# Kernel tuning notes

Measured on AMD Instinct MI355X. Metric: run time of the kernel, lower is better.

## Reference

```python
import jax, jax.numpy as jnp
import numpy as np

HIDDEN = 1024
N_HEAD = 16
LN_EPS = 1e-5


def _layernorm(x, g, b):
    m = jnp.mean(x, axis=-1, keepdims=True)
    v = jnp.var(x, axis=-1, keepdims=True)
    return (x - m) * jax.lax.rsqrt(v + LN_EPS) * g + b


def setup_inputs() -> dict:
    key = jax.random.key(0)
    ks = jax.random.split(key, 16)
    H = HIDDEN
    s = 0.02
    d = dict(
        x=jax.random.normal(ks[0], (4, 1024, H), jnp.float32),
        Wq=jax.random.normal(ks[1], (H, H), jnp.float32) * s,
        bq=jnp.zeros((H,), jnp.float32),
        Wk=jax.random.normal(ks[2], (H, H), jnp.float32) * s,
        bk=jnp.zeros((H,), jnp.float32),
        Wv=jax.random.normal(ks[3], (H, H), jnp.float32) * s,
        bv=jnp.zeros((H,), jnp.float32),
        Wo=jax.random.normal(ks[4], (H, H), jnp.float32) * s,
        bo=jnp.zeros((H,), jnp.float32),
        g1=jax.random.normal(ks[5], (H,), jnp.float32) * s,
        b1=jnp.zeros((H,), jnp.float32),
        W1=jax.random.normal(ks[6], (H, 4 * H), jnp.float32) * s,
        c1=jnp.zeros((4 * H,), jnp.float32),
        W2=jax.random.normal(ks[7], (4 * H, H), jnp.float32) * s,
        c2=jnp.zeros((H,), jnp.float32),
        g2=jax.random.normal(ks[8], (H,), jnp.float32) * s,
        b2=jnp.zeros((H,), jnp.float32),
    )
    return d


def reference(x, Wq, bq, Wk, bk, Wv, bv, Wo, bo, g1, b1, W1, c1, W2, c2, g2, b2):
    N, T, Hd = x.shape
    Hh = N_HEAD
    D = Hd // Hh
    # faithful to torch code: .view(N, H, T, D) is a raw reshape, no transpose
    q = (x @ Wq + bq).reshape(N, Hh, T, D)
    k = (x @ Wk + bk).reshape(N, Hh, T, D)
    v = (x @ Wv + bv).reshape(N, Hh, T, D)
    scores = jnp.einsum('nhtd,nhsd->nhts', q, k) / jnp.sqrt(jnp.float32(Hd))
    # faithful: softmax over dim=1 (the head axis)
    attn = jax.nn.softmax(scores, axis=1)
    o = jnp.einsum('nhts,nhsd->nhtd', attn, v).reshape(N, T, Hd)
    o = o @ Wo + bo
    x1 = _layernorm(o + x, g1, b1)
    ff = jax.nn.gelu(x1 @ W1 + c1, approximate=False) @ W2 + c2
    return _layernorm(ff + x1, g2, b2)
```

## Files before the change

kernel.cpp:

```cpp
#include <hip/hip_runtime.h>
#include <cstdint>
#include <cstddef>

#define EPI_QKV  0
#define EPI_F32  2
#define EPI_GELU 3
#define EPI_PART 4

typedef __attribute__((ext_vector_type(8))) short bfrag8;
typedef __attribute__((ext_vector_type(4))) float facc4;

struct PtrQuad { unsigned short* p[4]; };

__device__ __forceinline__ unsigned short f2b(float x) {
  unsigned int u = __builtin_bit_cast(unsigned int, x);
  u += 0x7FFFu + ((u >> 16) & 1u);
  return (unsigned short)(u >> 16);
}
__device__ __forceinline__ float b2f(unsigned short u) {
  unsigned int x = ((unsigned int)u) << 16;
  return __builtin_bit_cast(float, x);
}

__device__ __forceinline__ void gl2lds16(const unsigned short* g, unsigned short* l) {
  __builtin_amdgcn_global_load_lds(
      (const __attribute__((address_space(1))) unsigned int*)g,
      (__attribute__((address_space(3))) unsigned int*)l, 16, 0, 0);
}

__global__ __launch_bounds__(256)
void cvt_bf16_kernel(const float* __restrict__ in, unsigned short* __restrict__ out, int n4) {
  const int i = blockIdx.x * 256 + threadIdx.x;
  if (i < n4) {
    const float4 v = ((const float4*)in)[i];
    ushort4 u;
    u.x = f2b(v.x); u.y = f2b(v.y); u.z = f2b(v.z); u.w = f2b(v.w);
    ((ushort4*)out)[i] = u;
  }
}

__global__ __launch_bounds__(256)
void transpose_cvt(const float* __restrict__ in, unsigned short* __restrict__ out,
                   int K, int N) {
  __shared__ float tile[32][33];
  const int n0 = blockIdx.x * 32;
  const int k0 = blockIdx.y * 32;
  const int tx = threadIdx.x & 31, ty = threadIdx.x >> 5;
#pragma unroll
  for (int i = 0; i < 32; i += 8)
    tile[ty + i][tx] = in[(size_t)(k0 + ty + i) * N + n0 + tx];
  __syncthreads();
#pragma unroll
  for (int i = 0; i < 32; i += 8)
    out[(size_t)(n0 + ty + i) * K + k0 + tx] = f2b(tile[tx][ty + i]);
}

template<int EPI>
__global__ __launch_bounds__(256, 2)
void gemm_bt(const unsigned short* __restrict__ A,
             const unsigned short* __restrict__ Bt,
             const float* __restrict__ bias,
             const float* __restrict__ bias2,
             const float* __restrict__ bias3,
             void* __restrict__ out, PtrQuad pq,
             int M, int N, int K, int ldk) {
  __shared__ unsigned short sA[128 * 32];
  __shared__ unsigned short sB[128 * 32];
  const int tid  = threadIdx.x;
  const int lane = tid & 63;
  const int wave = tid >> 6;
  const int l15  = lane & 15, l4 = lane >> 4;
  const int wr = wave >> 1, wc = wave & 1;
  const long row0 = (long)blockIdx.y * 128;
  const long col0 = (long)blockIdx.x * 128;
  const long k0   = (long)blockIdx.z * K;

  facc4 acc[4][4];
#pragma unroll
  for (int i = 0; i < 4; i++)
#pragma unroll
    for (int j = 0; j < 4; j++) acc[i][j] = (facc4)0.f;

  const int srow = tid >> 2;
  const int scol = (tid & 3) * 8;
  const unsigned short* Ap0 = A  + (row0 + srow) * (long)ldk + k0 + scol;
  const unsigned short* Ap1 = Ap0 + 64 * (long)ldk;
  const unsigned short* Bp0 = Bt + (col0 + srow) * (long)ldk + k0 + scol;
  const unsigned short* Bp1 = Bp0 + 64 * (long)ldk;
  const int wbase = (tid & ~63) * 8;
  unsigned short* sA0 = &sA[wbase];
  unsigned short* sA1 = &sA[2048 + wbase];
  unsigned short* sB0 = &sB[wbase];
  unsigned short* sB1 = &sB[2048 + wbase];

  const int aoff = (wr * 64 + l15) * 32 + l4 * 8;
  const int boff = (wc * 64 + l15) * 32 + l4 * 8;

  for (int kt = 0; kt < K; kt += 32) {
    gl2lds16(Ap0 + kt, sA0);
    gl2lds16(Ap1 + kt, sA1);
    gl2lds16(Bp0 + kt, sB0);
    gl2lds16(Bp1 + kt, sB1);
    __syncthreads();
    bfrag8 af[4], bf[4];
#pragma unroll
    for (int i = 0; i < 4; i++) af[i] = *(const bfrag8*)&sA[aoff + i * 512];
#pragma unroll
    for (int j = 0; j < 4; j++) bf[j] = *(const bfrag8*)&sB[boff + j * 512];
#pragma unroll
    for (int i = 0; i < 4; i++)
#pragma unroll
      for (int j = 0; j < 4; j++)
        acc[i][j] = __builtin_amdgcn_mfma_f32_16x16x32_bf16(af[i], bf[j], acc[i][j], 0, 0, 0);
    __syncthreads();
  }

#pragma unroll
  for (int i = 0; i < 4; i++) {
    const long m0 = row0 + wr * 64 + i * 16 + l4 * 4;
#pragma unroll
    for (int j = 0; j < 4; j++) {
      const long c = col0 + wc * 64 + j * 16 + l15;
      if constexpr (EPI == EPI_QKV) {
        const long which = c >> 10;
        const long cl = c & 1023;
        unsigned short* oq = (unsigned short*)out;
        if (which == 0) {
          const float bj = bias[cl];
#pragma unroll
          for (int r = 0; r < 4; r++)
            oq[(m0 + r) * 1024 + cl] = f2b((acc[i][j][r] + bj) * 0.03125f);
        } else if (which == 1) {
          const float bj = bias2[cl];
#pragma unroll
          for (int r = 0; r < 4; r++)
            (oq + 4194304)[(m0 + r) * 1024 + cl] = f2b(acc[i][j][r] + bj);
        } else {
          const float bj = bias3[cl];
          const long cc = cl >> 6, d = cl & 63;
#pragma unroll
          for (int r = 0; r < 4; r++) {
            const long m = m0 + r;
            const long nbb = m >> 10, rr = m & 1023;
            const long h = rr >> 6, rhi = rr & 63;
            const long s = rhi * 16 + cc;
            (oq + 8388608)[((nbb * 16 + h) * 64 + d) * 1024 + s] = f2b(acc[i][j][r] + bj);
          }
        }
      } else if constexpr (EPI == EPI_F32) {
        const float bj = bias[c];
        float* of = (float*)out;
#pragma unroll
        for (int r = 0; r < 4; r++) of[(m0 + r) * (long)N + c] = acc[i][j][r] + bj;
      } else if constexpr (EPI == EPI_PART) {
        unsigned short* ob = pq.p[blockIdx.z];
#pragma unroll
        for (int r = 0; r < 4; r++) ob[(m0 + r) * (long)N + c] = f2b(acc[i][j][r]);
      } else {
        const float bj = bias[c];
        unsigned short* ob = (unsigned short*)out;
#pragma unroll
        for (int r = 0; r < 4; r++) {
          const float t = acc[i][j][r] + bj;
          ob[(m0 + r) * (long)N + c] = f2b(0.5f * t * (1.f + erff(t * 0.70710678f)));
        }
      }
    }
  }
}

__global__ __launch_bounds__(512, 1)
void attn_kernel(const unsigned short* __restrict__ Qb,
                 const unsigned short* __restrict__ Kb,
                 const unsigned short* __restrict__ Vt,
                 unsigned short* __restrict__ P0, unsigned short* __restrict__ P1) {
  const int id = blockIdx.x;
  const int combo = id & 7;
  const int nb = combo & 3;
  const int sp = combo >> 2;
  const int tile = id >> 3;
  const int tid = threadIdx.x, lane = tid & 63;
  const int w = __builtin_amdgcn_readfirstlane(tid >> 6);
  const int l15 = lane & 15, l4 = lane >> 4;
  const int t0 = tile * 32;
  const int sbase = sp * 512;
  const int h0 = w * 2;

  __shared__ __align__(16) float Ds[8][32][68];
  __shared__ __align__(16) float Dt[32][68];
  __shared__ __align__(16) unsigned short Pw[8][1024];

  const size_t bb = ((size_t)(nb * 16)) << 16;
  const unsigned short* qB = Qb + bb;
  const unsigned short* kB = Kb + bb;
  const unsigned short* vB = Vt + bb;

  bfrag8 qf[2][2][2];
#pragma unroll
  for (int hh = 0; hh < 2; hh++)
#pragma unroll
    for (int ts = 0; ts < 2; ts++)
#pragma unroll
      for (int dh = 0; dh < 2; dh++)
        qf[hh][ts][dh] = *(const bfrag8*)(qB + ((size_t)(h0 + hh) << 16)
            + (size_t)(t0 + ts * 16 + l15) * 64 + dh * 32 + l4 * 8);

  const int swz = (l15 & 7) << 4;
  char* pw = (char*)&Pw[w][0];
  const int pwrow = l15 * 128;
  const int ti1 = tid >> 4;
  const int si1 = (tid & 15) * 4;

  facc4 oacc[2][2][4];
#pragma unroll
  for (int hh = 0; hh < 2; hh++)
#pragma unroll
    for (int ts = 0; ts < 2; ts++)
#pragma unroll
      for (int nt = 0; nt < 4; nt++) oacc[hh][ts][nt] = (facc4)0.f;

  for (int it = 0; it < 8; ++it) {
    const int s0 = sbase + it * 64;
    bfrag8 kf[2][4][2];
#pragma unroll
    for (int hh = 0; hh < 2; hh++) {
      const unsigned short* kh_ = kB + ((size_t)(h0 + hh) << 16) + (size_t)l15 * 64 + l4 * 8;
#pragma unroll
      for (int ss = 0; ss < 4; ss++)
#pragma unroll
        for (int kh = 0; kh < 2; kh++)
          kf[hh][ss][kh] = *(const bfrag8*)(kh_ + (size_t)(s0 + ss * 16) * 64 + kh * 32);
    }
    facc4 sc[2][2][4];
#pragma unroll
    for (int hh = 0; hh < 2; hh++)
#pragma unroll
      for (int ts = 0; ts < 2; ts++)
#pragma unroll
        for (int ss = 0; ss < 4; ss++) {
          facc4 a = __builtin_amdgcn_mfma_f32_16x16x32_bf16(kf[hh][ss][0], qf[hh][ts][0],
                                                            (facc4)0.f, 0, 0, 0);
          sc[hh][ts][ss] = __builtin_amdgcn_mfma_f32_16x16x32_bf16(kf[hh][ss][1],
                                                                   qf[hh][ts][1], a, 0, 0, 0);
        }
    bfrag8 vf[2][2][4];
#pragma unroll
    for (int hh = 0; hh < 2; hh++) {
      const unsigned short* vh_ = vB + ((size_t)(h0 + hh) << 16) + (size_t)l15 * 1024 + s0 + l4 * 8;
#pragma unroll
      for (int sk = 0; sk < 2; sk++)
#pragma unroll
        for (int nt = 0; nt < 4; nt++)
          vf[hh][sk][nt] = *(const bfrag8*)(vh_ + (size_t)(nt * 16) * 1024 + sk * 32);
    }
    facc4 dacc[2][4];
#pragma unroll
    for (int ts = 0; ts < 2; ts++)
#pragma unroll
      for (int ss = 0; ss < 4; ss++) dacc[ts][ss] = (facc4)0.f;
#pragma unroll
    for (int hh = 0; hh < 2; hh++)
#pragma unroll
      for (int ts = 0; ts < 2; ts++)
#pragma unroll
        for (int ss = 0; ss < 4; ss++)
#pragma unroll
          for (int r = 0; r < 4; r++) {
            const float e = __expf(sc[hh][ts][ss][r]);
            sc[hh][ts][ss][r] = e;
            dacc[ts][ss][r] += e;
          }
#pragma unroll
    for (int ts = 0; ts < 2; ts++)
#pragma unroll
      for (int ss = 0; ss < 4; ss++)
        *(facc4*)&Ds[w][ts * 16 + l15][ss * 16 + l4 * 4] = dacc[ts][ss];
    __syncthreads();
    {
      facc4 s_ = *(const facc4*)&Ds[0][ti1][si1];
#pragma unroll
      for (int ww = 1; ww < 8; ww++) s_ += *(const facc4*)&Ds[ww][ti1][si1];
      *(facc4*)&Dt[ti1][si1] = s_;
    }
    __syncthreads();
    facc4 rt[2][4];
#pragma unroll
    for (int ts = 0; ts < 2; ts++)
#pragma unroll
      for (int ss = 0; ss < 4; ss++) {
        const facc4 d = *(const facc4*)&Dt[ts * 16 + l15][ss * 16 + l4 * 4];
#pragma unroll
        for (int r = 0; r < 4; r++) rt[ts][ss][r] = __builtin_amdgcn_rcpf(d[r]);
      }
#pragma unroll
    for (int hh = 0; hh < 2; hh++)
#pragma unroll
      for (int ts = 0; ts < 2; ts++) {
#pragma unroll
        for (int ss = 0; ss < 4; ss++) {
          const float p0 = sc[hh][ts][ss][0] * rt[ts][ss][0];
          const float p1 = sc[hh][ts][ss][1] * rt[ts][ss][1];
          const float p2 = sc[hh][ts][ss][2] * rt[ts][ss][2];
          const float p3 = sc[hh][ts][ss][3] * rt[ts][ss][3];
          uint2 pk;
          asm("v_cvt_pk_bf16_f32 %0, %1, %2" : "=v"(pk.x) : "v"(p0), "v"(p1));
          asm("v_cvt_pk_bf16_f32 %0, %1, %2" : "=v"(pk.y) : "v"(p2), "v"(p3));
          *(uint2*)(pw + pwrow + ((ss * 32 + l4 * 8) ^ swz)) = pk;
        }
        const bfrag8 a0 = *(const bfrag8*)(pw + pwrow + ((l4 * 16) ^ swz));
        const bfrag8 a1 = *(const bfrag8*)(pw + pwrow + ((64 + l4 * 16) ^ swz));
#pragma unroll
        for (int nt = 0; nt < 4; nt++) {
          oacc[hh][ts][nt] = __builtin_amdgcn_mfma_f32_16x16x32_bf16(a0, vf[hh][0][nt],
                                                                    oacc[hh][ts][nt], 0, 0, 0);
          oacc[hh][ts][nt] = __builtin_amdgcn_mfma_f32_16x16x32_bf16(a1, vf[hh][1][nt],
                                                                    oacc[hh][ts][nt], 0, 0, 0);
        }
      }
  }

  unsigned short* P = sp ? P1 : P0;
#pragma unroll
  for (int hh = 0; hh < 2; hh++) {
    const size_t hb = ((size_t)nb << 20) + ((size_t)(h0 + hh) << 16);
#pragma unroll
    for (int ts = 0; ts < 2; ts++)
#pragma unroll
      for (int nt = 0; nt < 4; nt++)
#pragma unroll
        for (int r = 0; r < 4; r++)
          P[hb + (size_t)(t0 + ts * 16 + l4 * 4 + r) * 64 + nt * 16 + l15] =
              f2b(oacc[hh][ts][nt][r]);
  }
}

__global__ __launch_bounds__(256)
void reduce_o2(const unsigned short* __restrict__ P0, const unsigned short* __restrict__ P1,
               unsigned short* __restrict__ OB, int n4) {
  const int i = blockIdx.x * 256 + threadIdx.x;
  if (i < n4) {
    const ushort4 a = ((const ushort4*)P0)[i];
    const ushort4 b = ((const ushort4*)P1)[i];
    ushort4 u;
    u.x = f2b(b2f(a.x) + b2f(b.x));
    u.y = f2b(b2f(a.y) + b2f(b.y));
    u.z = f2b(b2f(a.z) + b2f(b.z));
    u.w = f2b(b2f(a.w) + b2f(b.w));
    ((ushort4*)OB)[i] = u;
  }
}

__global__ __launch_bounds__(256)
void ln_red(const unsigned short* __restrict__ P0, const unsigned short* __restrict__ P1,
            const unsigned short* __restrict__ P2, const unsigned short* __restrict__ P3,
            const float* __restrict__ bias, const float* __restrict__ resid,
            const float* __restrict__ g, const float* __restrict__ be,
            float* __restrict__ outf, unsigned short* __restrict__ outb) {
  const int row = blockIdx.x, tid = threadIdx.x;
  const size_t o4 = (size_t)row * 256 + tid;
  const ushort4 a = ((const ushort4*)P0)[o4];
  const ushort4 b = ((const ushort4*)P1)[o4];
  const ushort4 c = ((const ushort4*)P2)[o4];
  const ushort4 d = ((const ushort4*)P3)[o4];
  const float4 vb = ((const float4*)bias)[tid];
  const float4 vr = ((const float4*)resid)[o4];
  float t0 = b2f(a.x) + b2f(b.x) + b2f(c.x) + b2f(d.x) + vb.x + vr.x;
  float t1 = b2f(a.y) + b2f(b.y) + b2f(c.y) + b2f(d.y) + vb.y + vr.y;
  float t2 = b2f(a.z) + b2f(b.z) + b2f(c.z) + b2f(d.z) + vb.z + vr.z;
  float t3 = b2f(a.w) + b2f(b.w) + b2f(c.w) + b2f(d.w) + vb.w + vr.w;
  float s = t0 + t1 + t2 + t3;
  float q = t0 * t0 + t1 * t1 + t2 * t2 + t3 * t3;
#pragma unroll
  for (int off = 32; off > 0; off >>= 1) {
    s += __shfl_down(s, off, 64);
    q += __shfl_down(q, off, 64);
  }
  __shared__ float rs_[4], rq_[4];
  if ((tid & 63) == 0) { rs_[tid >> 6] = s; rq_[tid >> 6] = q; }
  __syncthreads();
  const float S = rs_[0] + rs_[1] + rs_[2] + rs_[3];
  const float Q = rq_[0] + rq_[1] + rq_[2] + rq_[3];
  const float mean = S * (1.f / 1024.f);
  const float var  = Q * (1.f / 1024.f) - mean * mean;
  const float rstd = rsqrtf(var + 1e-5f);
  const float4 vg  = ((const float4*)g)[tid];
  const float4 vbe = ((const float4*)be)[tid];
  float o0 = (t0 - mean) * rstd * vg.x + vbe.x;
  float o1 = (t1 - mean) * rstd * vg.y + vbe.y;
  float o2 = (t2 - mean) * rstd * vg.z + vbe.z;
  float o3 = (t3 - mean) * rstd * vg.w + vbe.w;
  ((float4*)(outf + (size_t)row * 1024))[tid] = make_float4(o0, o1, o2, o3);
  if (outb != nullptr) {
    ushort4 u;
    u.x = f2b(o0); u.y = f2b(o1); u.z = f2b(o2); u.w = f2b(o3);
    ((ushort4*)(outb + (size_t)row * 1024))[tid] = u;
  }
}

extern "C" void kernel_launch(void* const* d_in, const int* in_sizes, int n_in,
                              void* d_out, int out_size, void* d_ws, size_t ws_size,
                              hipStream_t stream) {
  const float* x  = (const float*)d_in[0];
  const float* Wq = (const float*)d_in[1];
  const float* bq = (const float*)d_in[2];
  const float* Wk = (const float*)d_in[3];
  const float* bk = (const float*)d_in[4];
  const float* Wv = (const float*)d_in[5];
  const float* bv = (const float*)d_in[6];
  const float* Wo = (const float*)d_in[7];
  const float* bo = (const float*)d_in[8];
  const float* g1 = (const float*)d_in[9];
  const float* b1 = (const float*)d_in[10];
  const float* W1 = (const float*)d_in[11];
  const float* c1 = (const float*)d_in[12];
  const float* W2 = (const float*)d_in[13];
  const float* c2 = (const float*)d_in[14];
  const float* g2 = (const float*)d_in[15];
  const float* b2 = (const float*)d_in[16];
  float* out = (float*)d_out;

  char* ws = (char*)d_ws;
  unsigned short* XB  = (unsigned short*)(ws);
  unsigned short* WQT = (unsigned short*)(ws + 8388608);
  unsigned short* WKT = (unsigned short*)(ws + 10485760);
  unsigned short* WVT = (unsigned short*)(ws + 12582912);
  unsigned short* WOT = (unsigned short*)(ws + 14680064);
  unsigned short* W1T = (unsigned short*)(ws + 16777216);
  unsigned short* W2T = (unsigned short*)(ws + 25165824);
  float*          X1  = (float*)(ws + 33554432);
  unsigned short* X1B = (unsigned short*)(ws + 50331648);
  char* RB = ws + 58720256;
  unsigned short* QB  = (unsigned short*)(RB);
  unsigned short* KB  = (unsigned short*)(RB + 8388608);
  unsigned short* VT  = (unsigned short*)(RB + 16777216);
  unsigned short* OB  = (unsigned short*)(RB + 25165824);
  unsigned short* H1B = (unsigned short*)(RB);
  unsigned short* AP0 = (unsigned short*)(RB + 33554432);
  unsigned short* AP1 = (unsigned short*)(RB + 41943040);
  PtrQuad OPQ = { { QB, KB, VT, XB } };
  PtrQuad FPQ = { { XB, X1B, (unsigned short*)(RB + 33554432),
                    (unsigned short*)(RB + 41943040) } };
  PtrQuad ZQ = { { nullptr, nullptr, nullptr, nullptr } };

  const dim3 tb(256);
  cvt_bf16_kernel<<<dim3(4096), tb, 0, stream>>>(x, XB, 1048576);
  transpose_cvt<<<dim3(32, 32),  tb, 0, stream>>>(Wq, WQT, 1024, 1024);
  transpose_cvt<<<dim3(32, 32),  tb, 0, stream>>>(Wk, WKT, 1024, 1024);
  transpose_cvt<<<dim3(32, 32),  tb, 0, stream>>>(Wv, WVT, 1024, 1024);
  transpose_cvt<<<dim3(32, 32),  tb, 0, stream>>>(Wo, WOT, 1024, 1024);
  transpose_cvt<<<dim3(128, 32), tb, 0, stream>>>(W1, W1T, 1024, 4096);
  transpose_cvt<<<dim3(32, 128), tb, 0, stream>>>(W2, W2T, 4096, 1024);
  gemm_bt<EPI_QKV><<<dim3(24, 32), tb, 0, stream>>>(XB, WQT, bq, bk, bv, (void*)QB, ZQ,
                                                    4096, 3072, 1024, 1024);
  attn_kernel<<<dim3(256), dim3(512), 0, stream>>>(QB, KB, VT, AP0, AP1);
  reduce_o2<<<dim3(4096), tb, 0, stream>>>(AP0, AP1, OB, 1048576);
  gemm_bt<EPI_PART><<<dim3(8, 32, 4), tb, 0, stream>>>(OB, WOT, nullptr, nullptr, nullptr,
                                                       nullptr, OPQ, 4096, 1024, 256, 1024);
  ln_red<<<dim3(4096), tb, 0, stream>>>(QB, KB, VT, XB, bo, x, g1, b1, X1, X1B);
  gemm_bt<EPI_GELU><<<dim3(32, 32), tb, 0, stream>>>(X1B, W1T, c1, nullptr, nullptr,
                                                     (void*)H1B, ZQ, 4096, 4096, 1024, 1024);
  gemm_bt<EPI_PART><<<dim3(8, 32, 4), tb, 0, stream>>>(H1B, W2T, nullptr, nullptr, nullptr,
                                                       nullptr, FPQ, 4096, 1024, 1024, 4096);
  ln_red<<<dim3(4096), tb, 0, stream>>>(FPQ.p[0], FPQ.p[1], FPQ.p[2], FPQ.p[3], c2, X1,
                                        g2, b2, out, (unsigned short*)nullptr);
}
```

Before: 428.8 us.

## Split attention key range four ways and alias P staging into score LDS

The attention kernel now splits the key/sequence range into four chunks of 256 instead of two of 512, doubling the grid to 512 blocks. Partial outputs go to four buffers and are summed by a four-way reduction kernel. The per-warp P staging buffer is moved into the existing Ds shared array, cutting LDS use so more blocks may fit per CU. The cost is extra partial-output traffic in the reduction and extra bf16 rounding. Aliasing Pw onto Ds is only safe if that Ds region is no longer live when P is written.

```diff
diff --git a/kernel.cpp b/kernel.cpp
--- a/kernel.cpp
+++ b/kernel.cpp
@@ -173,22 +173,21 @@
 void attn_kernel(const unsigned short* __restrict__ Qb,
                  const unsigned short* __restrict__ Kb,
                  const unsigned short* __restrict__ Vt,
-                 unsigned short* __restrict__ P0, unsigned short* __restrict__ P1) {
+                 PtrQuad APQ) {
   const int id = blockIdx.x;
-  const int combo = id & 7;
+  const int combo = id & 15;
   const int nb = combo & 3;
   const int sp = combo >> 2;
-  const int tile = id >> 3;
+  const int tile = id >> 4;
   const int tid = threadIdx.x, lane = tid & 63;
   const int w = __builtin_amdgcn_readfirstlane(tid >> 6);
   const int l15 = lane & 15, l4 = lane >> 4;
   const int t0 = tile * 32;
-  const int sbase = sp * 512;
+  const int sbase = sp * 256;
   const int h0 = w * 2;
 
   __shared__ __align__(16) float Ds[8][32][68];
   __shared__ __align__(16) float Dt[32][68];
-  __shared__ __align__(16) unsigned short Pw[8][1024];
 
   const size_t bb = ((size_t)(nb * 16)) << 16;
   const unsigned short* qB = Qb + bb;
@@ -206,7 +205,7 @@
             + (size_t)(t0 + ts * 16 + l15) * 64 + dh * 32 + l4 * 8);
 
   const int swz = (l15 & 7) << 4;
-  char* pw = (char*)&Pw[w][0];
+  char* pw = (char*)&Ds[w][0][0];
   const int pwrow = l15 * 128;
   const int ti1 = tid >> 4;
   const int si1 = (tid & 15) * 4;
@@ -219,7 +218,7 @@
 #pragma unroll
       for (int nt = 0; nt < 4; nt++) oacc[hh][ts][nt] = (facc4)0.f;
 
-  for (int it = 0; it < 8; ++it) {
+  for (int it = 0; it < 4; ++it) {
     const int s0 = sbase + it * 64;
     bfrag8 kf[2][4][2];
 #pragma unroll
@@ -319,7 +318,7 @@
       }
   }
 
-  unsigned short* P = sp ? P1 : P0;
+  unsigned short* P = APQ.p[sp];
 #pragma unroll
   for (int hh = 0; hh < 2; hh++) {
     const size_t hb = ((size_t)nb << 20) + ((size_t)(h0 + hh) << 16);
@@ -335,17 +334,18 @@
 }
 
 __global__ __launch_bounds__(256)
-void reduce_o2(const unsigned short* __restrict__ P0, const unsigned short* __restrict__ P1,
-               unsigned short* __restrict__ OB, int n4) {
+void reduce_o4(PtrQuad pq, unsigned short* __restrict__ OB, int n4) {
   const int i = blockIdx.x * 256 + threadIdx.x;
   if (i < n4) {
-    const ushort4 a = ((const ushort4*)P0)[i];
-    const ushort4 b = ((const ushort4*)P1)[i];
+    const ushort4 a = ((const ushort4*)pq.p[0])[i];
+    const ushort4 b = ((const ushort4*)pq.p[1])[i];
+    const ushort4 c = ((const ushort4*)pq.p[2])[i];
+    const ushort4 d = ((const ushort4*)pq.p[3])[i];
     ushort4 u;
-    u.x = f2b(b2f(a.x) + b2f(b.x));
-    u.y = f2b(b2f(a.y) + b2f(b.y));
-    u.z = f2b(b2f(a.z) + b2f(b.z));
-    u.w = f2b(b2f(a.w) + b2f(b.w));
+    u.x = f2b(b2f(a.x) + b2f(b.x) + b2f(c.x) + b2f(d.x));
+    u.y = f2b(b2f(a.y) + b2f(b.y) + b2f(c.y) + b2f(d.y));
+    u.z = f2b(b2f(a.z) + b2f(b.z) + b2f(c.z) + b2f(d.z));
+    u.w = f2b(b2f(a.w) + b2f(b.w) + b2f(c.w) + b2f(d.w));
     ((ushort4*)OB)[i] = u;
   }
 }
@@ -437,6 +437,9 @@
   unsigned short* H1B = (unsigned short*)(RB);
   unsigned short* AP0 = (unsigned short*)(RB + 33554432);
   unsigned short* AP1 = (unsigned short*)(RB + 41943040);
+  unsigned short* AP2 = (unsigned short*)(ws + 33554432);
+  unsigned short* AP3 = (unsigned short*)(ws + 41943040);
+  PtrQuad APQ = { { AP0, AP1, AP2, AP3 } };
   PtrQuad OPQ = { { QB, KB, VT, XB } };
   PtrQuad FPQ = { { XB, X1B, (unsigned short*)(RB + 33554432),
                     (unsigned short*)(RB + 41943040) } };
@@ -452,8 +455,8 @@
   transpose_cvt<<<dim3(32, 128), tb, 0, stream>>>(W2, W2T, 4096, 1024);
   gemm_bt<EPI_QKV><<<dim3(24, 32), tb, 0, stream>>>(XB, WQT, bq, bk, bv, (void*)QB, ZQ,
                                                     4096, 3072, 1024, 1024);
-  attn_kernel<<<dim3(256), dim3(512), 0, stream>>>(QB, KB, VT, AP0, AP1);
-  reduce_o2<<<dim3(4096), tb, 0, stream>>>(AP0, AP1, OB, 1048576);
+  attn_kernel<<<dim3(512), dim3(512), 0, stream>>>(QB, KB, VT, APQ);
+  reduce_o4<<<dim3(4096), tb, 0, stream>>>(APQ, OB, 1048576);
   gemm_bt<EPI_PART><<<dim3(8, 32, 4), tb, 0, stream>>>(OB, WOT, nullptr, nullptr, nullptr,
                                                        nullptr, OPQ, 4096, 1024, 256, 1024);
   ln_red<<<dim3(4096), tb, 0, stream>>>(QB, KB, VT, XB, bo, x, g1, b1, X1, X1B);
```

Result: no change. 421.8 us (-1.6%).
